# Kernel tuning notes

Measured on AMD Instinct MI355X. Metric: run time of the kernel, lower is better.

Reference implementation:

```python
import jax, jax.numpy as jnp
import numpy as np

NUM_VARS = 10
HID = 256
INP = 4
B = 32
T = 64

_adj = np.ones((NUM_VARS, NUM_VARS)) - np.eye(NUM_VARS)
SEND, RECV = np.where(_adj)          # each [E], E = num_vars*(num_vars-1) = 90
E = len(SEND)
_e2n = np.zeros((NUM_VARS, E), dtype=np.float32)
_e2n[RECV, np.arange(E)] = 1.0       # encode_onehot(recv).T -> [num_vars, E]
E2N = jnp.asarray(_e2n)
SEND_J = jnp.asarray(SEND)
RECV_J = jnp.asarray(RECV)


def _mlp_block(x, w1, b1, w2, b2, gamma, beta):
    # RefNRIMLP: elu(fc1) -> (dropout p=0) -> elu(fc2) -> batchnorm over view(-1, H)
    h = jax.nn.elu(x @ w1 + b1)
    h = jax.nn.elu(h @ w2 + b2)
    mu = h.mean(axis=(0, 1, 2), keepdims=True)
    var = h.var(axis=(0, 1, 2), keepdims=True)
    return gamma * (h - mu) * jax.lax.rsqrt(var + 1e-5) + beta


def setup_inputs() -> dict:
    key = jax.random.key(0)
    ks = jax.random.split(key, 12)

    def xavier(k, fi, fo):
        return jax.random.normal(k, (fi, fo), jnp.float32) * np.sqrt(2.0 / (fi + fo))

    d = {
        "x": jax.random.normal(ks[0], (B, T, NUM_VARS, INP), jnp.float32),
        # mlp1: inp -> hid -> hid
        "w1a": xavier(ks[1], INP, HID), "b1a": jnp.full((HID,), 0.1),
        "w1b": xavier(ks[2], HID, HID), "b1b": jnp.full((HID,), 0.1),
        "g1": jnp.ones((HID,)), "be1": jnp.zeros((HID,)),
        # mlp2: 2*hid -> hid -> hid
        "w2a": xavier(ks[3], 2 * HID, HID), "b2a": jnp.full((HID,), 0.1),
        "w2b": xavier(ks[4], HID, HID), "b2b": jnp.full((HID,), 0.1),
        "g2": jnp.ones((HID,)), "be2": jnp.zeros((HID,)),
        # mlp3: hid -> hid -> hid
        "w3a": xavier(ks[5], HID, HID), "b3a": jnp.full((HID,), 0.1),
        "w3b": xavier(ks[6], HID, HID), "b3b": jnp.full((HID,), 0.1),
        "g3": jnp.ones((HID,)), "be3": jnp.zeros((HID,)),
        # output heads
        "wo1": xavier(ks[7], HID, HID), "bo1": jnp.full((HID,), 0.1),
        "wo2": xavier(ks[8], HID, 1), "bo2": jnp.full((1,), 0.1),
    }
    return d


def reference(x, w1a, b1a, w1b, b1b, g1, be1,
              w2a, b2a, w2b, b2b, g2, be2,
              w3a, b3a, w3b, b3b, g3, be3,
              wo1, bo1, wo2, bo2):
    # x: [B, T, N, INP] -> transpose(2,1): [B, N, T, INP]
    h = jnp.transpose(x, (0, 2, 1, 3))
    h = _mlp_block(h, w1a, b1a, w1b, b1b, g1, be1)            # [B, N, T, H]
    # node2edge: gather senders/receivers along node dim, concat on features
    e = jnp.concatenate([h[:, SEND_J], h[:, RECV_J]], axis=-1)  # [B, E, T, 2H]
    e = _mlp_block(e, w2a, b2a, w2b, b2b, g2, be2)            # [B, E, T, H]
    # edge2node: incidence matmul over edge dim, normalize by in-degree
    n = jnp.einsum('ve,betH->bvtH', E2N, e) / (NUM_VARS - 1)   # [B, N, T, H]
    n = _mlp_block(n, w3a, b3a, w3b, b3b, g3, be3)
    n = jax.nn.relu(n) @ wo1 + bo1
    n = jax.nn.relu(n) @ wo2 + bo2                             # [B, N, T, 1]
    out = jnp.transpose(n, (0, 2, 1, 3)).mean(axis=-1)         # [B, T, N]
    return out
```

## Files before the change

### kernel.cpp

```cpp
#include <hip/hip_runtime.h>
#include <hip/hip_bf16.h>
#include <cstdint>

#define DI __device__ __forceinline__

typedef short bf16x8 __attribute__((ext_vector_type(8)));
typedef float f32x4 __attribute__((ext_vector_type(4)));
typedef unsigned short u16;
typedef unsigned short u16x8 __attribute__((ext_vector_type(8)));

static constexpr int NV = 10, NE = 90, TT = 64;
static constexpr int R1 = 20480;
static constexpr int R2 = 184320;

DI float bf2f(u16 u) { union { unsigned int i; float f; } x; x.i = ((unsigned int)u) << 16; return x.f; }
DI u16 f2bf(float f) { unsigned int u = __float_as_uint(f); return (u16)((u + 0x7FFF + ((u >> 16) & 1)) >> 16); }
DI float elu(float v) { return v > 0.f ? v : __expf(v) - 1.f; }

#define GLL(srcp, dstp) __builtin_amdgcn_global_load_lds( \
    (const __attribute__((address_space(1))) unsigned int*)(srcp), \
    (__attribute__((address_space(3))) unsigned int*)(dstp), 16, 0, 0)

__global__ __launch_bounds__(256) void pack4(
    const float* __restrict__ s0, u16* __restrict__ d0,
    const float* __restrict__ s1, u16* __restrict__ d1,
    const float* __restrict__ s2, u16* __restrict__ d2,
    const float* __restrict__ s3, u16* __restrict__ d3) {
    const float* s; u16* d;
    switch (blockIdx.y) {
        case 0: s = s0; d = d0; break;
        case 1: s = s1; d = d1; break;
        case 2: s = s2; d = d2; break;
        default: s = s3; d = d3; break;
    }
    int tid = threadIdx.x;
    int bn = blockIdx.x >> 3, kt = blockIdx.x & 7;
#pragma unroll
    for (int p = 0; p < 2; ++p) {
        int n = bn * 128 + p * 64 + (tid >> 2);
        int k = kt * 32 + (tid & 3) * 8;
        u16x8 pk;
#pragma unroll
        for (int e = 0; e < 8; ++e) pk[e] = f2bf(s[(size_t)(k + e) * 256 + n]);
        *(u16x8*)(d + ((size_t)((bn * 8 + kt) * 2 + p)) * 2048 + (size_t)tid * 8) = pk;
    }
}

__global__ __launch_bounds__(256) void pack256(const float* __restrict__ s,
                                               u16* __restrict__ d) {
    int kt = blockIdx.x;
#pragma unroll
    for (int h = 0; h < 2; ++h) {
        int tid2 = threadIdx.x + h * 256;
#pragma unroll
        for (int p = 0; p < 2; ++p) {
            int n = p * 128 + (tid2 >> 2);
            int k = kt * 32 + (tid2 & 3) * 8;
            u16x8 pk;
#pragma unroll
            for (int e = 0; e < 8; ++e) pk[e] = f2bf(s[(size_t)(k + e) * 256 + n]);
            *(u16x8*)(d + ((size_t)(kt * 2 + p)) * 4096 + (size_t)tid2 * 8) = pk;
        }
    }
}

__global__ __launch_bounds__(256) void pack256_w2a(const float* __restrict__ w2a,
                                                   const float* __restrict__ scsh1,
                                                   u16* __restrict__ d) {
    int kt = blockIdx.x;
#pragma unroll
    for (int h = 0; h < 2; ++h) {
        int tid2 = threadIdx.x + h * 256;
#pragma unroll
        for (int p = 0; p < 2; ++p) {
            int n = p * 128 + (tid2 >> 2);
            int k = kt * 32 + (tid2 & 3) * 8;
            u16x8 pk;
#pragma unroll
            for (int e = 0; e < 8; ++e)
                pk[e] = f2bf(scsh1[(k + e) & 255] * w2a[(size_t)(k + e) * 256 + n]);
            *(u16x8*)(d + ((size_t)(kt * 2 + p)) * 4096 + (size_t)tid2 * 8) = pk;
        }
    }
}

__global__ void zero_stats(float* p, int n) {
    int i = blockIdx.x * 256 + threadIdx.x;
    if (i < n) p[i] = 0.f;
}

__global__ void conv_wo2(const float* __restrict__ src, u16* __restrict__ dst) {
    dst[threadIdx.x] = f2bf(src[threadIdx.x]);
}

__global__ __launch_bounds__(256) void fold_b2a(const float* __restrict__ w2a,
                                                const float* __restrict__ scsh1,
                                                const float* __restrict__ b2a,
                                                float* __restrict__ b2aF) {
    __shared__ float red[256];
    int n = blockIdx.x, tid = threadIdx.x;
    float sc = scsh1[256 + tid];
    float s = sc * w2a[tid * 256 + n] + sc * w2a[(tid + 256) * 256 + n];
    red[tid] = s;
    __syncthreads();
    for (int off2 = 128; off2 > 0; off2 >>= 1) {
        if (tid < off2) red[tid] += red[tid + off2];
        __syncthreads();
    }
    if (tid == 0) b2aF[n] = red[0] + b2a[n];
}

__global__ void stats_final(const float* __restrict__ sums, const float* __restrict__ g,
                            const float* __restrict__ be, float invR, float* __restrict__ scsh) {
    int c = threadIdx.x;
    float mu = sums[c] * invR;
    float var = sums[256 + c] * invR - mu * mu;
    float rs = rsqrtf(var + 1e-5f);
    float sc = g[c] * rs;
    scsh[c] = sc;
    scsh[256 + c] = be[c] - mu * sc;
}

__global__ __launch_bounds__(256) void mlp1_fc1(const float* __restrict__ x,
                                                const float* __restrict__ w1a,
                                                const float* __restrict__ b1a,
                                                u16* __restrict__ ha) {
    int tid = threadIdx.x;
    int row = blockIdx.x * 8 + (tid >> 5);
    int ch8 = (tid & 31) * 8;
    int b = row / (NV * TT);
    int v = (row >> 6) % NV;
    int t = row & 63;
    const float* xp = x + ((size_t)(b * TT + t) * NV + v) * 4;
    float x0 = xp[0], x1 = xp[1], x2 = xp[2], x3 = xp[3];
    u16x8 pack;
#pragma unroll
    for (int e = 0; e < 8; ++e) {
        int c = ch8 + e;
        float acc = b1a[c] + x0 * w1a[c] + x1 * w1a[256 + c] + x2 * w1a[512 + c] + x3 * w1a[768 + c];
        pack[e] = f2bf(elu(acc));
    }
    *(u16x8*)(ha + (size_t)row * 256 + ch8) = pack;
}

template <int ACT, bool STATS>
__global__ __launch_bounds__(256) void gemm_kernel(const u16* __restrict__ A,
                                                   const u16* __restrict__ Wt,
                                                   const float* __restrict__ bias,
                                                   u16* __restrict__ out,
                                                   int K,
                                                   float* __restrict__ stats) {
    __shared__ u16 As[3][128 * 32];
    __shared__ u16 Bs[3][128 * 32];
    const int tid = threadIdx.x;
    const int lane = tid & 63, wid = tid >> 6;

    int bm, bn;
    {
        int bid = blockIdx.x;
        int xcd = bid & 7, slot = bid >> 3;
        bn = slot & 1;
        bm = xcd + 8 * (slot >> 1);
    }
    const int m0 = bm * 128, n0 = bn * 128;
    const int wm = wid >> 1, wn = wid & 1;

    const int srow = tid >> 2;
    const int scol8 = (tid & 3) * 8;

    size_t abase0 = (size_t)(m0 + srow) * K;
    size_t abase1 = (size_t)(m0 + srow + 64) * K;
    const int NT = K >> 5;
    const size_t bnbase = (size_t)bn * NT * 4096;

    f32x4 acc[4][4];
#pragma unroll
    for (int i = 0; i < 4; ++i)
#pragma unroll
        for (int j = 0; j < 4; ++j) acc[i][j] = (f32x4)0.f;

    const int lrow = lane & 15;
    const int lk8 = (lane >> 4) * 8;

    auto stage = [&](int bf, int k0) {
        const size_t btile = bnbase + (size_t)(k0 >> 5) * 4096 + (size_t)tid * 8;
        GLL(A + abase0 + k0 + scol8, &As[bf][(wid * 64) * 8]);
        GLL(Wt + btile, &Bs[bf][(wid * 64) * 8]);
        GLL(A + abase1 + k0 + scol8, &As[bf][(256 + wid * 64) * 8]);
        GLL(Wt + btile + 2048, &Bs[bf][(256 + wid * 64) * 8]);
    };

    stage(0, 0);
    stage(1, 32);
    for (int kt = 0; kt < NT; ++kt) {
        if (kt + 1 < NT) {
            asm volatile("s_waitcnt vmcnt(4)" ::: "memory");
        } else {
            asm volatile("s_waitcnt vmcnt(0)" ::: "memory");
        }
        __builtin_amdgcn_s_barrier();
        if (kt + 2 < NT) stage((kt + 2) % 3, (kt + 2) * 32);
        __builtin_amdgcn_sched_barrier(0);
        const int buf = kt % 3;
        bf16x8 a[4], b[4];
#pragma unroll
        for (int i = 0; i < 4; ++i)
            a[i] = *(const bf16x8*)&As[buf][(wm * 64 + i * 16 + lrow) * 32 + lk8];
#pragma unroll
        for (int j = 0; j < 4; ++j)
            b[j] = *(const bf16x8*)&Bs[buf][(wn * 64 + j * 16 + lrow) * 32 + lk8];
#pragma unroll
        for (int i = 0; i < 4; ++i)
#pragma unroll
            for (int j = 0; j < 4; ++j)
                acc[i][j] = __builtin_amdgcn_mfma_f32_16x16x32_bf16(a[i], b[j], acc[i][j], 0, 0, 0);
    }

    float bv[4], sv[4], qv[4];
#pragma unroll
    for (int j = 0; j < 4; ++j) {
        bv[j] = bias[n0 + wn * 64 + j * 16 + lrow];
        if constexpr (STATS) { sv[j] = 0.f; qv[j] = 0.f; }
    }
#pragma unroll
    for (int i = 0; i < 4; ++i) {
#pragma unroll
        for (int j = 0; j < 4; ++j) {
            int col = n0 + wn * 64 + j * 16 + lrow;
#pragma unroll
            for (int r = 0; r < 4; ++r) {
                int row = m0 + wm * 64 + i * 16 + (lane >> 4) * 4 + r;
                float v = acc[i][j][r] + bv[j];
                v = (ACT == 1) ? elu(v) : (v > 0.f ? v : 0.f);
                if constexpr (STATS) { sv[j] += v; qv[j] += v * v; }
                out[(size_t)row * 256 + col] = f2bf(v);
            }
        }
    }
    if constexpr (STATS) {
#pragma unroll
        for (int j = 0; j < 4; ++j) {
            float s = sv[j], q_ = qv[j];
            s += __shfl_xor(s, 16); q_ += __shfl_xor(q_, 16);
            s += __shfl_xor(s, 32); q_ += __shfl_xor(q_, 32);
            if ((lane >> 4) == 0) {
                int col = n0 + wn * 64 + j * 16 + lrow;
                atomicAdd(&stats[col], s);
                atomicAdd(&stats[256 + col], q_);
            }
        }
    }
}

template <bool GATHER, bool STATS>
__global__ __launch_bounds__(512) void gemm256(const u16* __restrict__ A,
                                               const u16* __restrict__ PK,
                                               const float* __restrict__ bias,
                                               u16* __restrict__ out,
                                               int K,
                                               float* __restrict__ stats) {
    __shared__ u16 As[3][256 * 32];
    __shared__ u16 Bs[3][256 * 32];
    const int tid = threadIdx.x;
    const int lane = tid & 63, wid = tid >> 6;

    const int bm = (blockIdx.x & 7) * 90 + (blockIdx.x >> 3);
    const int m0 = bm * 256;
    const int wm = wid >> 2, wn = wid & 3;

    const int srow = tid >> 2;
    const int scol8 = (tid & 3) * 8;

    size_t ab0 = 0, ab1 = 0, sb0 = 0, sb1 = 0, rb0 = 0, rb1 = 0;
    if constexpr (GATHER) {
        {
            int m = m0 + srow;
            int t = m & 63, be = m >> 6, e = be % NE, b = be / NE;
            int s = e / 9, kk = e - s * 9, r = kk + (kk >= s ? 1 : 0);
            sb0 = ((size_t)((b * NV + s) * TT + t)) * 256;
            rb0 = ((size_t)((b * NV + r) * TT + t)) * 256;
        }
        {
            int m = m0 + srow + 128;
            int t = m & 63, be = m >> 6, e = be % NE, b = be / NE;
            int s = e / 9, kk = e - s * 9, r = kk + (kk >= s ? 1 : 0);
            sb1 = ((size_t)((b * NV + s) * TT + t)) * 256;
            rb1 = ((size_t)((b * NV + r) * TT + t)) * 256;
        }
    } else {
        ab0 = (size_t)(m0 + srow) * K;
        ab1 = (size_t)(m0 + srow + 128) * K;
    }
    const int NT = K >> 5;

    f32x4 acc[8][4];
#pragma unroll
    for (int i = 0; i < 8; ++i)
#pragma unroll
        for (int j = 0; j < 4; ++j) acc[i][j] = (f32x4)0.f;

    const int lrow = lane & 15;
    const int lk8 = (lane >> 4) * 8;

    auto stage = [&](int bf, int k0) {
        const size_t btile = (size_t)(k0 >> 5) * 8192 + (size_t)tid * 8;
        const u16 *a0, *a1;
        if constexpr (GATHER) {
            int f = k0 + scol8;
            a0 = A + (f < 256 ? sb0 + f : rb0 + (f - 256));
            a1 = A + (f < 256 ? sb1 + f : rb1 + (f - 256));
        } else {
            a0 = A + ab0 + k0 + scol8;
            a1 = A + ab1 + k0 + scol8;
        }
        GLL(a0, &As[bf][tid * 8]);
        GLL(PK + btile, &Bs[bf][tid * 8]);
        GLL(a1, &As[bf][4096 + tid * 8]);
        GLL(PK + btile + 4096, &Bs[bf][4096 + tid * 8]);
    };

    stage(0, 0);
    stage(1, 32);
    for (int kt = 0; kt < NT; ++kt) {
        if (kt + 1 < NT) {
            asm volatile("s_waitcnt vmcnt(4)" ::: "memory");
        } else {
            asm volatile("s_waitcnt vmcnt(0)" ::: "memory");
        }
        __builtin_amdgcn_s_barrier();
        if (kt + 2 < NT) stage((kt + 2) % 3, (kt + 2) * 32);
        __builtin_amdgcn_sched_barrier(0);
        const int buf = kt % 3;
        bf16x8 a[8], b[4];
#pragma unroll
        for (int i = 0; i < 8; ++i)
            a[i] = *(const bf16x8*)&As[buf][(wm * 128 + i * 16 + lrow) * 32 + lk8];
#pragma unroll
        for (int j = 0; j < 4; ++j)
            b[j] = *(const bf16x8*)&Bs[buf][(wn * 64 + j * 16 + lrow) * 32 + lk8];
#pragma unroll
        for (int i = 0; i < 8; ++i)
#pragma unroll
            for (int j = 0; j < 4; ++j)
                acc[i][j] = __builtin_amdgcn_mfma_f32_16x16x32_bf16(a[i], b[j], acc[i][j], 0, 0, 0);
    }

    float bv[4], sv[4], qv[4];
#pragma unroll
    for (int j = 0; j < 4; ++j) {
        bv[j] = bias[wn * 64 + j * 16 + lrow];
        if constexpr (STATS) { sv[j] = 0.f; qv[j] = 0.f; }
    }
#pragma unroll
    for (int i = 0; i < 8; ++i) {
#pragma unroll
        for (int j = 0; j < 4; ++j) {
            int col = wn * 64 + j * 16 + lrow;
#pragma unroll
            for (int r = 0; r < 4; ++r) {
                int row = m0 + wm * 128 + i * 16 + (lane >> 4) * 4 + r;
                float v = acc[i][j][r] + bv[j];
                v = elu(v);
                if constexpr (STATS) { sv[j] += v; qv[j] += v * v; }
                out[(size_t)row * 256 + col] = f2bf(v);
            }
        }
    }
    if constexpr (STATS) {
#pragma unroll
        for (int j = 0; j < 4; ++j) {
            float s = sv[j], q_ = qv[j];
            s += __shfl_xor(s, 16); q_ += __shfl_xor(q_, 16);
            s += __shfl_xor(s, 32); q_ += __shfl_xor(q_, 32);
            if ((lane >> 4) == 0) {
                int col = wn * 64 + j * 16 + lrow;
                atomicAdd(&stats[col], s);
                atomicAdd(&stats[256 + col], q_);
            }
        }
    }
}

__global__ __launch_bounds__(256) void norm_affine_relu(const u16* __restrict__ in,
                                                        const float* __restrict__ scsh,
                                                        u16* __restrict__ out, int n8) {
    int i = blockIdx.x * 256 + threadIdx.x;
    if (i >= n8) return;
    size_t base = (size_t)i * 8;
    int ch8 = (int)(base & 255);
    u16x8 v = *(const u16x8*)(in + base);
    u16x8 o;
#pragma unroll
    for (int e = 0; e < 8; ++e) {
        float f = bf2f(v[e]);
        f = scsh[ch8 + e] * f + scsh[256 + ch8 + e];
        o[e] = f2bf(f > 0.f ? f : 0.f);
    }
    *(u16x8*)(out + base) = o;
}

__global__ __launch_bounds__(256) void edge2node(const u16* __restrict__ h2,
                                                 const float* __restrict__ scsh2,
                                                 u16* __restrict__ n1) {
    int tid = threadIdx.x;
    int row = blockIdx.x * 8 + (tid >> 5);
    int ch8 = (tid & 31) * 8;
    int t = row & 63;
    int bv = row >> 6;
    int v = bv % NV;
    int b = bv / NV;
    float acc[8] = {0, 0, 0, 0, 0, 0, 0, 0};
#pragma unroll
    for (int i = 0; i < 9; ++i) {
        int s = i + (i >= v ? 1 : 0);
        int e = s * 9 + (v < s ? v : v - 1);
        u16x8 vv = *(const u16x8*)(h2 + ((size_t)((b * NE + e) * TT + t)) * 256 + ch8);
#pragma unroll
        for (int k = 0; k < 8; ++k) acc[k] += bf2f(vv[k]);
    }
    const float inv9 = 1.f / 9.f;
    u16x8 o;
#pragma unroll
    for (int k = 0; k < 8; ++k) {
        int c = ch8 + k;
        o[k] = f2bf(scsh2[c] * (acc[k] * inv9) + scsh2[256 + c]);
    }
    *(u16x8*)(n1 + (size_t)row * 256 + ch8) = o;
}

__global__ __launch_bounds__(256) void head2(const u16* __restrict__ a2,
                                             const u16* __restrict__ wo2t,
                                             const float* __restrict__ bo2,
                                             float* __restrict__ out) {
    int tid = threadIdx.x;
    int row = blockIdx.x * 8 + (tid >> 5);
    int l32 = tid & 31;
    int ch8 = l32 * 8;
    u16x8 a = *(const u16x8*)(a2 + (size_t)row * 256 + ch8);
    u16x8 w = *(const u16x8*)(wo2t + ch8);
    float p = 0.f;
#pragma unroll
    for (int k = 0; k < 8; ++k) p += bf2f(a[k]) * bf2f(w[k]);
#pragma unroll
    for (int off = 16; off > 0; off >>= 1) p += __shfl_down(p, off, 32);
    if (l32 == 0) {
        int b = row / (NV * TT);
        int v = (row >> 6) % NV;
        int t = row & 63;
        out[(size_t)(b * TT + t) * NV + v] = p + bo2[0];
    }
}

extern "C" void kernel_launch(void* const* d_in, const int* in_sizes, int n_in,
                              void* d_out, int out_size, void* d_ws, size_t ws_size,
                              hipStream_t stream) {
    const float* x   = (const float*)d_in[0];
    const float* w1a = (const float*)d_in[1];
    const float* b1a = (const float*)d_in[2];
    const float* w1b = (const float*)d_in[3];
    const float* b1b = (const float*)d_in[4];
    const float* g1  = (const float*)d_in[5];
    const float* be1 = (const float*)d_in[6];
    const float* w2a = (const float*)d_in[7];
    const float* b2a = (const float*)d_in[8];
    const float* w2b = (const float*)d_in[9];
    const float* b2b = (const float*)d_in[10];
    const float* g2  = (const float*)d_in[11];
    const float* be2 = (const float*)d_in[12];
    const float* w3a = (const float*)d_in[13];
    const float* b3a = (const float*)d_in[14];
    const float* w3b = (const float*)d_in[15];
    const float* b3b = (const float*)d_in[16];
    const float* g3  = (const float*)d_in[17];
    const float* be3 = (const float*)d_in[18];
    const float* wo1 = (const float*)d_in[19];
    const float* bo1 = (const float*)d_in[20];
    const float* wo2 = (const float*)d_in[21];
    const float* bo2 = (const float*)d_in[22];
    float* out = (float*)d_out;

    char* ws = (char*)d_ws;
    size_t off = 0;
    auto alloc = [&](size_t bytes) {
        void* p = ws + off;
        off = (off + bytes + 255) & ~(size_t)255;
        return p;
    };
    u16* w1bP = (u16*)alloc(2 * 8 * 4096 * 2);
    u16* w3aP = (u16*)alloc(2 * 8 * 4096 * 2);
    u16* w3bP = (u16*)alloc(2 * 8 * 4096 * 2);
    u16* wo1P = (u16*)alloc(2 * 8 * 4096 * 2);
    u16* w2aP = (u16*)alloc(16 * 8192 * 2);
    u16* w2bP = (u16*)alloc(8 * 8192 * 2);
    u16* wo2T = (u16*)alloc(256 * 2);
    float* sums  = (float*)alloc(3 * 512 * 4);
    float* scsh1 = (float*)alloc(512 * 4);
    float* scsh2 = (float*)alloc(512 * 4);
    float* scsh3 = (float*)alloc(512 * 4);
    float* b2aF  = (float*)alloc(256 * 4);
    u16* S0 = (u16*)alloc((size_t)R1 * 256 * 2);
    u16* S1 = (u16*)alloc((size_t)R1 * 256 * 2);
    u16* S2 = (u16*)alloc((size_t)R1 * 256 * 2);
    u16* BIG1 = (u16*)alloc((size_t)R2 * 256 * 2);
    u16* BIG2 = (u16*)alloc((size_t)R2 * 256 * 2);

    dim3 pgrid(16, 4);
    pack4<<<pgrid, 256, 0, stream>>>(w1b, w1bP, w3a, w3aP, w3b, w3bP, wo1, wo1P);
    pack256<<<8, 256, 0, stream>>>(w2b, w2bP);
    zero_stats<<<6, 256, 0, stream>>>(sums, 3 * 512);
    conv_wo2<<<1, 256, 0, stream>>>(wo2, wo2T);

    mlp1_fc1<<<R1 / 8, 256, 0, stream>>>(x, w1a, b1a, S0);
    gemm_kernel<1, true><<<(R1 / 128) * 2, 256, 0, stream>>>(S0, w1bP, b1b, S1, 256, sums);
    stats_final<<<1, 256, 0, stream>>>(sums, g1, be1, 1.f / R1, scsh1);
    pack256_w2a<<<16, 256, 0, stream>>>(w2a, scsh1, w2aP);
    fold_b2a<<<256, 256, 0, stream>>>(w2a, scsh1, b2a, b2aF);

    gemm256<true, false><<<R2 / 256, 512, 0, stream>>>(S1, w2aP, b2aF, BIG1, 512, nullptr);
    gemm256<false, true><<<R2 / 256, 512, 0, stream>>>(BIG1, w2bP, b2b, BIG2, 256, sums + 512);
    stats_final<<<1, 256, 0, stream>>>(sums + 512, g2, be2, 1.f / R2, scsh2);

    edge2node<<<R1 / 8, 256, 0, stream>>>(BIG2, scsh2, S0);

    gemm_kernel<1, false><<<(R1 / 128) * 2, 256, 0, stream>>>(S0, w3aP, b3a, S1, 256, nullptr);
    gemm_kernel<1, true><<<(R1 / 128) * 2, 256, 0, stream>>>(S1, w3bP, b3b, S2, 256, sums + 1024);
    stats_final<<<1, 256, 0, stream>>>(sums + 1024, g3, be3, 1.f / R1, scsh3);

    norm_affine_relu<<<(R1 * 32 + 255) / 256, 256, 0, stream>>>(S2, scsh3, S0, R1 * 32);
    gemm_kernel<2, false><<<(R1 / 128) * 2, 256, 0, stream>>>(S0, wo1P, bo1, S1, 256, nullptr);
    head2<<<R1 / 8, 256, 0, stream>>>(S1, wo2T, bo2, out);
}
```

Before: 266.3 us.

## Switch edge GEMMs to 32x32x16 MFMA with 4 waves and swizzled LDS

The two large edge-MLP GEMMs move from 8 waves doing 16x16x32 MFMAs on 128x64 sub-tiles to 4 waves doing 32x32x16 MFMAs on 128x128 sub-tiles. The weight packing and the A-tile staging now apply an XOR swizzle on the 8-element k-groups, which should reduce LDS bank conflicts on the fragment reads. Larger MFMA tiles cut LDS read traffic per FLOP and lower the instruction count. In exchange there are fewer waves per block and more accumulator registers per thread (256 floats), which can limit latency hiding or cause spills.

```diff
diff --git a/kernel.cpp b/kernel.cpp
--- a/kernel.cpp
+++ b/kernel.cpp
@@ -6,6 +6,7 @@
 
 typedef short bf16x8 __attribute__((ext_vector_type(8)));
 typedef float f32x4 __attribute__((ext_vector_type(4)));
+typedef float f32x16 __attribute__((ext_vector_type(16)));
 typedef unsigned short u16;
 typedef unsigned short u16x8 __attribute__((ext_vector_type(8)));
 
@@ -46,41 +47,37 @@
     }
 }
 
-__global__ __launch_bounds__(256) void pack256(const float* __restrict__ s,
-                                               u16* __restrict__ d) {
+__global__ __launch_bounds__(256) void pack256s(const float* __restrict__ s,
+                                                u16* __restrict__ d) {
     int kt = blockIdx.x;
 #pragma unroll
-    for (int h = 0; h < 2; ++h) {
+    for (int h = 0; h < 4; ++h) {
         int tid2 = threadIdx.x + h * 256;
-#pragma unroll
-        for (int p = 0; p < 2; ++p) {
-            int n = p * 128 + (tid2 >> 2);
-            int k = kt * 32 + (tid2 & 3) * 8;
-            u16x8 pk;
-#pragma unroll
-            for (int e = 0; e < 8; ++e) pk[e] = f2bf(s[(size_t)(k + e) * 256 + n]);
-            *(u16x8*)(d + ((size_t)(kt * 2 + p)) * 4096 + (size_t)tid2 * 8) = pk;
-        }
-    }
-}
-
-__global__ __launch_bounds__(256) void pack256_w2a(const float* __restrict__ w2a,
-                                                   const float* __restrict__ scsh1,
-                                                   u16* __restrict__ d) {
+        int n = tid2 >> 2;
+        int g = (tid2 & 3) ^ ((tid2 >> 2) & 3);
+        int k = kt * 32 + g * 8;
+        u16x8 pk;
+#pragma unroll
+        for (int e = 0; e < 8; ++e) pk[e] = f2bf(s[(size_t)(k + e) * 256 + n]);
+        *(u16x8*)(d + (size_t)kt * 8192 + (size_t)tid2 * 8) = pk;
+    }
+}
+
+__global__ __launch_bounds__(256) void pack256s_w2a(const float* __restrict__ w2a,
+                                                    const float* __restrict__ scsh1,
+                                                    u16* __restrict__ d) {
     int kt = blockIdx.x;
 #pragma unroll
-    for (int h = 0; h < 2; ++h) {
+    for (int h = 0; h < 4; ++h) {
         int tid2 = threadIdx.x + h * 256;
-#pragma unroll
-        for (int p = 0; p < 2; ++p) {
-            int n = p * 128 + (tid2 >> 2);
-            int k = kt * 32 + (tid2 & 3) * 8;
-            u16x8 pk;
-#pragma unroll
-            for (int e = 0; e < 8; ++e)
-                pk[e] = f2bf(scsh1[(k + e) & 255] * w2a[(size_t)(k + e) * 256 + n]);
-            *(u16x8*)(d + ((size_t)(kt * 2 + p)) * 4096 + (size_t)tid2 * 8) = pk;
-        }
+        int n = tid2 >> 2;
+        int g = (tid2 & 3) ^ ((tid2 >> 2) & 3);
+        int k = kt * 32 + g * 8;
+        u16x8 pk;
+#pragma unroll
+        for (int e = 0; e < 8; ++e)
+            pk[e] = f2bf(scsh1[(k + e) & 255] * w2a[(size_t)(k + e) * 256 + n]);
+        *(u16x8*)(d + (size_t)kt * 8192 + (size_t)tid2 * 8) = pk;
     }
 }
 
@@ -253,12 +250,12 @@
 }
 
 template <bool GATHER, bool STATS>
-__global__ __launch_bounds__(512) void gemm256(const u16* __restrict__ A,
-                                               const u16* __restrict__ PK,
-                                               const float* __restrict__ bias,
-                                               u16* __restrict__ out,
-                                               int K,
-                                               float* __restrict__ stats) {
+__global__ __launch_bounds__(256) void gemm256b(const u16* __restrict__ A,
+                                                const u16* __restrict__ PK,
+                                                const float* __restrict__ bias,
+                                                u16* __restrict__ out,
+                                                int K,
+                                                float* __restrict__ stats) {
     __shared__ u16 As[3][256 * 32];
     __shared__ u16 Bs[3][256 * 32];
     const int tid = threadIdx.x;
@@ -266,64 +263,57 @@
 
     const int bm = (blockIdx.x & 7) * 90 + (blockIdx.x >> 3);
     const int m0 = bm * 256;
-    const int wm = wid >> 2, wn = wid & 3;
+    const int wm = wid >> 1, wn = wid & 1;
 
     const int srow = tid >> 2;
-    const int scol8 = (tid & 3) * 8;
-
-    size_t ab0 = 0, ab1 = 0, sb0 = 0, sb1 = 0, rb0 = 0, rb1 = 0;
+    const int sswz = ((tid & 3) ^ ((tid >> 2) & 3)) * 8;
+
+    size_t ab[4], sb[4], rb[4];
     if constexpr (GATHER) {
-        {
-            int m = m0 + srow;
+#pragma unroll
+        for (int q = 0; q < 4; ++q) {
+            int m = m0 + q * 64 + srow;
             int t = m & 63, be = m >> 6, e = be % NE, b = be / NE;
             int s = e / 9, kk = e - s * 9, r = kk + (kk >= s ? 1 : 0);
-            sb0 = ((size_t)((b * NV + s) * TT + t)) * 256;
-            rb0 = ((size_t)((b * NV + r) * TT + t)) * 256;
-        }
-        {
-            int m = m0 + srow + 128;
-            int t = m & 63, be = m >> 6, e = be % NE, b = be / NE;
-            int s = e / 9, kk = e - s * 9, r = kk + (kk >= s ? 1 : 0);
-            sb1 = ((size_t)((b * NV + s) * TT + t)) * 256;
-            rb1 = ((size_t)((b * NV + r) * TT + t)) * 256;
+            sb[q] = ((size_t)((b * NV + s) * TT + t)) * 256;
+            rb[q] = ((size_t)((b * NV + r) * TT + t)) * 256;
         }
     } else {
-        ab0 = (size_t)(m0 + srow) * K;
-        ab1 = (size_t)(m0 + srow + 128) * K;
+#pragma unroll
+        for (int q = 0; q < 4; ++q) ab[q] = (size_t)(m0 + q * 64 + srow) * K;
     }
     const int NT = K >> 5;
 
-    f32x4 acc[8][4];
-#pragma unroll
-    for (int i = 0; i < 8; ++i)
-#pragma unroll
-        for (int j = 0; j < 4; ++j) acc[i][j] = (f32x4)0.f;
-
-    const int lrow = lane & 15;
-    const int lk8 = (lane >> 4) * 8;
+    f32x16 acc[4][4];
+#pragma unroll
+    for (int bi = 0; bi < 4; ++bi)
+#pragma unroll
+        for (int bj = 0; bj < 4; ++bj) acc[bi][bj] = (f32x16)0.f;
 
     auto stage = [&](int bf, int k0) {
-        const size_t btile = (size_t)(k0 >> 5) * 8192 + (size_t)tid * 8;
-        const u16 *a0, *a1;
-        if constexpr (GATHER) {
-            int f = k0 + scol8;
-            a0 = A + (f < 256 ? sb0 + f : rb0 + (f - 256));
-            a1 = A + (f < 256 ? sb1 + f : rb1 + (f - 256));
-        } else {
-            a0 = A + ab0 + k0 + scol8;
-            a1 = A + ab1 + k0 + scol8;
-        }
-        GLL(a0, &As[bf][tid * 8]);
-        GLL(PK + btile, &Bs[bf][tid * 8]);
-        GLL(a1, &As[bf][4096 + tid * 8]);
-        GLL(PK + btile + 4096, &Bs[bf][4096 + tid * 8]);
+        const size_t btile = (size_t)(k0 >> 5) * 8192;
+#pragma unroll
+        for (int q = 0; q < 4; ++q) {
+            const u16* a_;
+            if constexpr (GATHER) {
+                a_ = A + (k0 < 256 ? sb[q] : rb[q]) + (k0 & 255) + sswz;
+            } else {
+                a_ = A + ab[q] + k0 + sswz;
+            }
+            GLL(a_, &As[bf][q * 2048 + wid * 512]);
+            GLL(PK + btile + q * 2048 + (size_t)tid * 8, &Bs[bf][q * 2048 + wid * 512]);
+        }
     };
+
+    const int l31 = lane & 31;
+    const int lh = lane >> 5;
+    const int lx = lane & 3;
 
     stage(0, 0);
     stage(1, 32);
     for (int kt = 0; kt < NT; ++kt) {
         if (kt + 1 < NT) {
-            asm volatile("s_waitcnt vmcnt(4)" ::: "memory");
+            asm volatile("s_waitcnt vmcnt(8)" ::: "memory");
         } else {
             asm volatile("s_waitcnt vmcnt(0)" ::: "memory");
         }
@@ -331,51 +321,51 @@
         if (kt + 2 < NT) stage((kt + 2) % 3, (kt + 2) * 32);
         __builtin_amdgcn_sched_barrier(0);
         const int buf = kt % 3;
-        bf16x8 a[8], b[4];
-#pragma unroll
-        for (int i = 0; i < 8; ++i)
-            a[i] = *(const bf16x8*)&As[buf][(wm * 128 + i * 16 + lrow) * 32 + lk8];
-#pragma unroll
-        for (int j = 0; j < 4; ++j)
-            b[j] = *(const bf16x8*)&Bs[buf][(wn * 64 + j * 16 + lrow) * 32 + lk8];
-#pragma unroll
-        for (int i = 0; i < 8; ++i)
-#pragma unroll
-            for (int j = 0; j < 4; ++j)
-                acc[i][j] = __builtin_amdgcn_mfma_f32_16x16x32_bf16(a[i], b[j], acc[i][j], 0, 0, 0);
-    }
-
-    float bv[4], sv[4], qv[4];
-#pragma unroll
-    for (int j = 0; j < 4; ++j) {
-        bv[j] = bias[wn * 64 + j * 16 + lrow];
-        if constexpr (STATS) { sv[j] = 0.f; qv[j] = 0.f; }
-    }
-#pragma unroll
-    for (int i = 0; i < 8; ++i) {
-#pragma unroll
-        for (int j = 0; j < 4; ++j) {
-            int col = wn * 64 + j * 16 + lrow;
-#pragma unroll
-            for (int r = 0; r < 4; ++r) {
-                int row = m0 + wm * 128 + i * 16 + (lane >> 4) * 4 + r;
-                float v = acc[i][j][r] + bv[j];
+#pragma unroll
+        for (int kk = 0; kk < 2; ++kk) {
+            const int g = (kk * 2 + lh) ^ lx;
+            bf16x8 a[4], b[4];
+#pragma unroll
+            for (int bi = 0; bi < 4; ++bi) {
+                int r = wm * 128 + bi * 32 + l31;
+                a[bi] = *(const bf16x8*)&As[buf][r * 32 + g * 8];
+            }
+#pragma unroll
+            for (int bj = 0; bj < 4; ++bj) {
+                int rn = wn * 128 + bj * 32 + l31;
+                b[bj] = *(const bf16x8*)&Bs[buf][rn * 32 + g * 8];
+            }
+#pragma unroll
+            for (int bi = 0; bi < 4; ++bi)
+#pragma unroll
+                for (int bj = 0; bj < 4; ++bj)
+                    acc[bi][bj] = __builtin_amdgcn_mfma_f32_32x32x16_bf16(a[bi], b[bj], acc[bi][bj], 0, 0, 0);
+        }
+    }
+
+#pragma unroll
+    for (int bj = 0; bj < 4; ++bj) {
+        int col = wn * 128 + bj * 32 + l31;
+        float bv = bias[col];
+        float sv = 0.f, qv = 0.f;
+#pragma unroll
+        for (int bi = 0; bi < 4; ++bi) {
+            int rbase = m0 + wm * 128 + bi * 32 + 4 * lh;
+#pragma unroll
+            for (int reg = 0; reg < 16; ++reg) {
+                int row = rbase + (reg & 3) + 8 * (reg >> 2);
+                float v = acc[bi][bj][reg] + bv;
                 v = elu(v);
-                if constexpr (STATS) { sv[j] += v; qv[j] += v * v; }
+                if constexpr (STATS) { sv += v; qv += v * v; }
                 out[(size_t)row * 256 + col] = f2bf(v);
             }
         }
-    }
-    if constexpr (STATS) {
-#pragma unroll
-        for (int j = 0; j < 4; ++j) {
-            float s = sv[j], q_ = qv[j];
-            s += __shfl_xor(s, 16); q_ += __shfl_xor(q_, 16);
-            s += __shfl_xor(s, 32); q_ += __shfl_xor(q_, 32);
-            if ((lane >> 4) == 0) {
-                int col = wn * 64 + j * 16 + lrow;
-                atomicAdd(&stats[col], s);
-                atomicAdd(&stats[256 + col], q_);
+        if constexpr (STATS) {
+            sv += __shfl_xor(sv, 32);
+            qv += __shfl_xor(qv, 32);
+            if (lh == 0) {
+                atomicAdd(&stats[col], sv);
+                atomicAdd(&stats[256 + col], qv);
             }
         }
     }
@@ -506,18 +496,18 @@
 
     dim3 pgrid(16, 4);
     pack4<<<pgrid, 256, 0, stream>>>(w1b, w1bP, w3a, w3aP, w3b, w3bP, wo1, wo1P);
-    pack256<<<8, 256, 0, stream>>>(w2b, w2bP);
+    pack256s<<<8, 256, 0, stream>>>(w2b, w2bP);
     zero_stats<<<6, 256, 0, stream>>>(sums, 3 * 512);
     conv_wo2<<<1, 256, 0, stream>>>(wo2, wo2T);
 
     mlp1_fc1<<<R1 / 8, 256, 0, stream>>>(x, w1a, b1a, S0);
     gemm_kernel<1, true><<<(R1 / 128) * 2, 256, 0, stream>>>(S0, w1bP, b1b, S1, 256, sums);
     stats_final<<<1, 256, 0, stream>>>(sums, g1, be1, 1.f / R1, scsh1);
-    pack256_w2a<<<16, 256, 0, stream>>>(w2a, scsh1, w2aP);
+    pack256s_w2a<<<16, 256, 0, stream>>>(w2a, scsh1, w2aP);
     fold_b2a<<<256, 256, 0, stream>>>(w2a, scsh1, b2a, b2aF);
 
-    gemm256<true, false><<<R2 / 256, 512, 0, stream>>>(S1, w2aP, b2aF, BIG1, 512, nullptr);
-    gemm256<false, true><<<R2 / 256, 512, 0, stream>>>(BIG1, w2bP, b2b, BIG2, 256, sums + 512);
+    gemm256b<true, false><<<R2 / 256, 256, 0, stream>>>(S1, w2aP, b2aF, BIG1, 512, nullptr);
+    gemm256b<false, true><<<R2 / 256, 256, 0, stream>>>(BIG1, w2bP, b2b, BIG2, 256, sums + 512);
     stats_final<<<1, 256, 0, stream>>>(sums + 512, g2, be2, 1.f / R2, scsh2);
 
     edge2node<<<R1 / 8, 256, 0, stream>>>(BIG2, scsh2, S0);
```

Measured after the change: 308.3 us. +15.8%, slower.

## Fuse mlp2 fc1 and fc2 GEMMs into one kernel keeping hidden tile in LDS

Applied to the files above, without the earlier changes.

Replaces the two back-to-back 256-row GEMM launches for the edge MLP with one fused kernel that computes a 128-row tile of fc1 (with the sender/receiver gather), applies ELU, and stores the result in a swizzled LDS buffer. It then runs fc2 directly from LDS, removing the round trip of the large intermediate edge activation through global memory and freeing that buffer. The block tile shrinks to 128 rows, so the weight tiles are reloaded twice as often per row. The block-to-tile mapping is also changed to group tiles per XCD by batch. LDS use rises to roughly 104KB per block, which lowers occupancy.

```diff
diff --git a/kernel.cpp b/kernel.cpp
--- a/kernel.cpp
+++ b/kernel.cpp
@@ -252,131 +252,168 @@
     }
 }
 
-template <bool GATHER, bool STATS>
-__global__ __launch_bounds__(512) void gemm256(const u16* __restrict__ A,
-                                               const u16* __restrict__ PK,
-                                               const float* __restrict__ bias,
-                                               u16* __restrict__ out,
-                                               int K,
-                                               float* __restrict__ stats) {
-    __shared__ u16 As[3][256 * 32];
+__global__ __launch_bounds__(512) void mlp2_fused(const u16* __restrict__ A,
+                                                  const u16* __restrict__ PB1,
+                                                  const float* __restrict__ bias1,
+                                                  const u16* __restrict__ PB2,
+                                                  const float* __restrict__ bias2,
+                                                  u16* __restrict__ out,
+                                                  float* __restrict__ stats) {
+    __shared__ u16 As[3][128 * 32];
     __shared__ u16 Bs[3][256 * 32];
+    __shared__ u16 H1[128 * 256];
+
     const int tid = threadIdx.x;
     const int lane = tid & 63, wid = tid >> 6;
 
-    const int bm = (blockIdx.x & 7) * 90 + (blockIdx.x >> 3);
-    const int m0 = bm * 256;
+    int bid = blockIdx.x;
+    int xcd = bid & 7, slot = bid >> 3;
+    int batch = xcd + 8 * (slot / 45);
+    int bm = batch * 45 + (slot % 45);
+    const int m0 = bm * 128;
     const int wm = wid >> 2, wn = wid & 3;
 
-    const int srow = tid >> 2;
-    const int scol8 = (tid & 3) * 8;
-
-    size_t ab0 = 0, ab1 = 0, sb0 = 0, sb1 = 0, rb0 = 0, rb1 = 0;
-    if constexpr (GATHER) {
-        {
-            int m = m0 + srow;
-            int t = m & 63, be = m >> 6, e = be % NE, b = be / NE;
-            int s = e / 9, kk = e - s * 9, r = kk + (kk >= s ? 1 : 0);
-            sb0 = ((size_t)((b * NV + s) * TT + t)) * 256;
-            rb0 = ((size_t)((b * NV + r) * TT + t)) * 256;
-        }
-        {
-            int m = m0 + srow + 128;
-            int t = m & 63, be = m >> 6, e = be % NE, b = be / NE;
-            int s = e / 9, kk = e - s * 9, r = kk + (kk >= s ? 1 : 0);
-            sb1 = ((size_t)((b * NV + s) * TT + t)) * 256;
-            rb1 = ((size_t)((b * NV + r) * TT + t)) * 256;
-        }
-    } else {
-        ab0 = (size_t)(m0 + srow) * K;
-        ab1 = (size_t)(m0 + srow + 128) * K;
-    }
-    const int NT = K >> 5;
-
-    f32x4 acc[8][4];
-#pragma unroll
-    for (int i = 0; i < 8; ++i)
-#pragma unroll
-        for (int j = 0; j < 4; ++j) acc[i][j] = (f32x4)0.f;
+    size_t sb, rb;
+    {
+        int m = m0 + (tid >> 2);
+        int t = m & 63, be = m >> 6, e = be % NE, b = be / NE;
+        int s = e / 9, kk = e - s * 9, r = kk + (kk >= s ? 1 : 0);
+        sb = ((size_t)((b * NV + s) * TT + t)) * 256 + (tid & 3) * 8;
+        rb = ((size_t)((b * NV + r) * TT + t)) * 256 + (tid & 3) * 8;
+    }
 
     const int lrow = lane & 15;
     const int lk8 = (lane >> 4) * 8;
 
-    auto stage = [&](int bf, int k0) {
-        const size_t btile = (size_t)(k0 >> 5) * 8192 + (size_t)tid * 8;
-        const u16 *a0, *a1;
-        if constexpr (GATHER) {
-            int f = k0 + scol8;
-            a0 = A + (f < 256 ? sb0 + f : rb0 + (f - 256));
-            a1 = A + (f < 256 ? sb1 + f : rb1 + (f - 256));
-        } else {
-            a0 = A + ab0 + k0 + scol8;
-            a1 = A + ab1 + k0 + scol8;
-        }
-        GLL(a0, &As[bf][tid * 8]);
-        GLL(PK + btile, &Bs[bf][tid * 8]);
-        GLL(a1, &As[bf][4096 + tid * 8]);
-        GLL(PK + btile + 4096, &Bs[bf][4096 + tid * 8]);
+    f32x4 acc[4][4];
+#pragma unroll
+    for (int i = 0; i < 4; ++i)
+#pragma unroll
+        for (int j = 0; j < 4; ++j) acc[i][j] = (f32x4)0.f;
+
+    auto stage1 = [&](int bf, int k0) {
+        GLL(A + (k0 < 256 ? sb : rb) + (k0 & 255), &As[bf][tid * 8]);
+        const u16* b_ = PB1 + (size_t)(k0 >> 5) * 8192 + (size_t)tid * 8;
+        GLL(b_, &Bs[bf][tid * 8]);
+        GLL(b_ + 4096, &Bs[bf][4096 + tid * 8]);
     };
 
-    stage(0, 0);
-    stage(1, 32);
-    for (int kt = 0; kt < NT; ++kt) {
-        if (kt + 1 < NT) {
-            asm volatile("s_waitcnt vmcnt(4)" ::: "memory");
+    stage1(0, 0);
+    stage1(1, 32);
+    for (int kt = 0; kt < 16; ++kt) {
+        if (kt + 1 < 16) {
+            asm volatile("s_waitcnt vmcnt(3)" ::: "memory");
         } else {
             asm volatile("s_waitcnt vmcnt(0)" ::: "memory");
         }
         __builtin_amdgcn_s_barrier();
-        if (kt + 2 < NT) stage((kt + 2) % 3, (kt + 2) * 32);
+        if (kt + 2 < 16) stage1((kt + 2) % 3, (kt + 2) * 32);
         __builtin_amdgcn_sched_barrier(0);
         const int buf = kt % 3;
-        bf16x8 a[8], b[4];
-#pragma unroll
-        for (int i = 0; i < 8; ++i)
-            a[i] = *(const bf16x8*)&As[buf][(wm * 128 + i * 16 + lrow) * 32 + lk8];
+        bf16x8 a[4], b[4];
+#pragma unroll
+        for (int i = 0; i < 4; ++i)
+            a[i] = *(const bf16x8*)&As[buf][(wm * 64 + i * 16 + lrow) * 32 + lk8];
 #pragma unroll
         for (int j = 0; j < 4; ++j)
             b[j] = *(const bf16x8*)&Bs[buf][(wn * 64 + j * 16 + lrow) * 32 + lk8];
 #pragma unroll
-        for (int i = 0; i < 8; ++i)
+        for (int i = 0; i < 4; ++i)
 #pragma unroll
             for (int j = 0; j < 4; ++j)
                 acc[i][j] = __builtin_amdgcn_mfma_f32_16x16x32_bf16(a[i], b[j], acc[i][j], 0, 0, 0);
     }
 
-    float bv[4], sv[4], qv[4];
 #pragma unroll
     for (int j = 0; j < 4; ++j) {
-        bv[j] = bias[wn * 64 + j * 16 + lrow];
-        if constexpr (STATS) { sv[j] = 0.f; qv[j] = 0.f; }
-    }
-#pragma unroll
-    for (int i = 0; i < 8; ++i) {
+        int c = wn * 64 + j * 16 + lrow;
+        float bv = bias1[c];
+        int gx = c >> 3;
+        int cl = c & 7;
+#pragma unroll
+        for (int i = 0; i < 4; ++i) {
+#pragma unroll
+            for (int r = 0; r < 4; ++r) {
+                int m = wm * 64 + i * 16 + (lane >> 4) * 4 + r;
+                float v = elu(acc[i][j][r] + bv);
+                H1[m * 256 + ((gx ^ (m & 7)) << 3) + cl] = f2bf(v);
+            }
+        }
+    }
+    __syncthreads();
+
+#pragma unroll
+    for (int i = 0; i < 4; ++i)
+#pragma unroll
+        for (int j = 0; j < 4; ++j) acc[i][j] = (f32x4)0.f;
+
+    auto stage2 = [&](int bf, int k0) {
+        const u16* b_ = PB2 + (size_t)(k0 >> 5) * 8192 + (size_t)tid * 8;
+        GLL(b_, &Bs[bf][tid * 8]);
+        GLL(b_ + 4096, &Bs[bf][4096 + tid * 8]);
+    };
+
+    stage2(0, 0);
+    stage2(1, 32);
+    for (int kt = 0; kt < 8; ++kt) {
+        if (kt + 1 < 8) {
+            asm volatile("s_waitcnt vmcnt(2)" ::: "memory");
+        } else {
+            asm volatile("s_waitcnt vmcnt(0)" ::: "memory");
+        }
+        __builtin_amdgcn_s_barrier();
+        if (kt + 2 < 8) stage2((kt + 2) % 3, (kt + 2) * 32);
+        __builtin_amdgcn_sched_barrier(0);
+        const int buf = kt % 3;
+        const int k0 = kt * 32;
+        bf16x8 a[4], b[4];
+#pragma unroll
+        for (int i = 0; i < 4; ++i) {
+            int mr = wm * 64 + i * 16 + lrow;
+            int gx = (k0 >> 3) + (lane >> 4);
+            a[i] = *(const bf16x8*)&H1[mr * 256 + ((gx ^ (mr & 7)) << 3)];
+        }
+#pragma unroll
+        for (int j = 0; j < 4; ++j)
+            b[j] = *(const bf16x8*)&Bs[buf][(wn * 64 + j * 16 + lrow) * 32 + lk8];
+#pragma unroll
+        for (int i = 0; i < 4; ++i)
+#pragma unroll
+            for (int j = 0; j < 4; ++j)
+                acc[i][j] = __builtin_amdgcn_mfma_f32_16x16x32_bf16(a[i], b[j], acc[i][j], 0, 0, 0);
+    }
+
+    float bv2[4], sv[4], qv[4];
+#pragma unroll
+    for (int j = 0; j < 4; ++j) {
+        bv2[j] = bias2[wn * 64 + j * 16 + lrow];
+        sv[j] = 0.f;
+        qv[j] = 0.f;
+    }
+#pragma unroll
+    for (int i = 0; i < 4; ++i) {
 #pragma unroll
         for (int j = 0; j < 4; ++j) {
             int col = wn * 64 + j * 16 + lrow;
 #pragma unroll
             for (int r = 0; r < 4; ++r) {
-                int row = m0 + wm * 128 + i * 16 + (lane >> 4) * 4 + r;
-                float v = acc[i][j][r] + bv[j];
-                v = elu(v);
-                if constexpr (STATS) { sv[j] += v; qv[j] += v * v; }
+                int row = m0 + wm * 64 + i * 16 + (lane >> 4) * 4 + r;
+                float v = elu(acc[i][j][r] + bv2[j]);
+                sv[j] += v;
+                qv[j] += v * v;
                 out[(size_t)row * 256 + col] = f2bf(v);
             }
         }
     }
-    if constexpr (STATS) {
-#pragma unroll
-        for (int j = 0; j < 4; ++j) {
-            float s = sv[j], q_ = qv[j];
-            s += __shfl_xor(s, 16); q_ += __shfl_xor(q_, 16);
-            s += __shfl_xor(s, 32); q_ += __shfl_xor(q_, 32);
-            if ((lane >> 4) == 0) {
-                int col = wn * 64 + j * 16 + lrow;
-                atomicAdd(&stats[col], s);
-                atomicAdd(&stats[256 + col], q_);
-            }
+#pragma unroll
+    for (int j = 0; j < 4; ++j) {
+        float s = sv[j], q_ = qv[j];
+        s += __shfl_xor(s, 16); q_ += __shfl_xor(q_, 16);
+        s += __shfl_xor(s, 32); q_ += __shfl_xor(q_, 32);
+        if ((lane >> 4) == 0) {
+            int col = wn * 64 + j * 16 + lrow;
+            atomicAdd(&stats[col], s);
+            atomicAdd(&stats[256 + col], q_);
         }
     }
 }
@@ -501,7 +538,6 @@
     u16* S0 = (u16*)alloc((size_t)R1 * 256 * 2);
     u16* S1 = (u16*)alloc((size_t)R1 * 256 * 2);
     u16* S2 = (u16*)alloc((size_t)R1 * 256 * 2);
-    u16* BIG1 = (u16*)alloc((size_t)R2 * 256 * 2);
     u16* BIG2 = (u16*)alloc((size_t)R2 * 256 * 2);
 
     dim3 pgrid(16, 4);
@@ -516,8 +552,7 @@
     pack256_w2a<<<16, 256, 0, stream>>>(w2a, scsh1, w2aP);
     fold_b2a<<<256, 256, 0, stream>>>(w2a, scsh1, b2a, b2aF);
 
-    gemm256<true, false><<<R2 / 256, 512, 0, stream>>>(S1, w2aP, b2aF, BIG1, 512, nullptr);
-    gemm256<false, true><<<R2 / 256, 512, 0, stream>>>(BIG1, w2bP, b2b, BIG2, 256, sums + 512);
+    mlp2_fused<<<R2 / 128, 512, 0, stream>>>(S1, w2aP, b2aF, w2bP, b2b, BIG2, sums + 512);
     stats_final<<<1, 256, 0, stream>>>(sums + 512, g2, be2, 1.f / R2, scsh2);
 
     edge2node<<<R1 / 8, 256, 0, stream>>>(BIG2, scsh2, S0);
```

New measurement: 244.9 us. 8.0% less time.
